# Kernel optimization log

Measured on AMD Instinct MI355X. Metric: run time of the kernel, lower is better.

## Reference

```python
import jax, jax.numpy as jnp
import numpy as np

SEQ_LEN = 8192
INPUT_SIZE = 1024
HIDDEN_SIZE = 2048


def setup_inputs() -> dict:
    key = jax.random.key(0)
    k_in, k_wz, k_wr, k_wh = jax.random.split(key, 4)
    concat = HIDDEN_SIZE + INPUT_SIZE
    return {
        "inputs": jax.random.normal(k_in, (SEQ_LEN, INPUT_SIZE), dtype=jnp.float32),
        "W_z": jax.random.normal(k_wz, (HIDDEN_SIZE, concat), dtype=jnp.float32) * 0.01,
        "b_z": jnp.zeros((HIDDEN_SIZE, 1), dtype=jnp.float32),
        "W_r": jax.random.normal(k_wr, (HIDDEN_SIZE, concat), dtype=jnp.float32) * 0.01,
        "b_r": jnp.zeros((HIDDEN_SIZE, 1), dtype=jnp.float32),
        "W_h": jax.random.normal(k_wh, (HIDDEN_SIZE, concat), dtype=jnp.float32) * 0.01,
        "b_h": jnp.zeros((HIDDEN_SIZE, 1), dtype=jnp.float32),
    }


def reference(inputs, W_z, b_z, W_r, b_r, W_h, b_h):
    # inputs: [T, I]; hidden state h: [H, 1] (batch size 1, column-vector form).
    H = W_z.shape[0]
    h0 = jnp.zeros((H, 1), dtype=inputs.dtype)

    def step(h_prev, x_t):
        x = x_t[:, None]  # [I, 1]
        concat = jnp.concatenate([h_prev, x], axis=0)  # [H+I, 1]
        z = jax.nn.sigmoid(W_z @ concat + b_z)
        r = jax.nn.sigmoid(W_r @ concat + b_r)
        concat_reset = jnp.concatenate([r * h_prev, x], axis=0)
        h_tilde = jnp.tanh(W_h @ concat_reset + b_h)
        h_t = (1.0 - z) * h_prev + z * h_tilde
        return h_t, h_t

    h_final, outputs = jax.lax.scan(step, h0, inputs)
    # outputs: [T, H, 1] (stack of the per-step hidden states the torch code collects in a list)
    return outputs, h_final
```

## Files before the change

kernel.cpp:

```cpp
#include <hip/hip_runtime.h>

#define SEQ  8192
#define HID  2048
#define INP  1024
#define CONC 3072
#define NBLK 256
#define RPB  8

typedef unsigned short u16;

__device__ __forceinline__ u16 f2bf(float f){
  unsigned u = __float_as_uint(f);
  u = (u + 0x7fffu + ((u >> 16) & 1u)) >> 16;
  return (u16)u;
}
__device__ __forceinline__ float bf2f(u16 s){ return __uint_as_float(((unsigned)s) << 16); }
__device__ __forceinline__ float bfl(unsigned p){ return __uint_as_float(p << 16); }
__device__ __forceinline__ float bfh(unsigned p){ return __uint_as_float(p & 0xffff0000u); }

__device__ __forceinline__ float cload(const float* p){
  return __hip_atomic_load(p, __ATOMIC_RELAXED, __HIP_MEMORY_SCOPE_AGENT);
}
__device__ __forceinline__ void cstore(float* p, float v){
  __hip_atomic_store(p, v, __ATOMIC_RELAXED, __HIP_MEMORY_SCOPE_AGENT);
}
__device__ __forceinline__ unsigned cloadu(const unsigned* p){
  return __hip_atomic_load(p, __ATOMIC_RELAXED, __HIP_MEMORY_SCOPE_AGENT);
}
__device__ __forceinline__ void cstoreu(unsigned* p, unsigned v){
  __hip_atomic_store(p, v, __ATOMIC_RELAXED, __HIP_MEMORY_SCOPE_AGENT);
}

__global__ __launch_bounds__(256) void gru_gemm(
    const float* __restrict__ X,
    const float* __restrict__ Wz, const float* __restrict__ Wr, const float* __restrict__ Wh,
    const float* __restrict__ bz, const float* __restrict__ br, const float* __restrict__ bh,
    u16* __restrict__ Uz, u16* __restrict__ Ur, u16* __restrict__ Uh)
{
  const int g = blockIdx.z;
  const float* W    = (g == 0) ? Wz : (g == 1) ? Wr : Wh;
  const float* bias = (g == 0) ? bz : (g == 1) ? br : bh;
  u16* U            = (g == 0) ? Uz : (g == 1) ? Ur : Uh;

  __shared__ __align__(16) float Xs[16][68];
  __shared__ __align__(16) float Ws[16][68];

  const int tid = threadIdx.x;
  const int tx = tid & 15, ty = tid >> 4;
  const int t0 = blockIdx.y * 64, i0 = blockIdx.x * 64;
  const int lrow = tid >> 2, lk = (tid & 3) * 4;

  const float* xsrc = X + (size_t)(t0 + lrow) * INP + lk;
  const float* wsrc = W + (size_t)(i0 + lrow) * CONC + HID + lk;

  float4 acc[4];
  acc[0] = acc[1] = acc[2] = acc[3] = make_float4(0.f, 0.f, 0.f, 0.f);

  for (int k0 = 0; k0 < INP; k0 += 16) {
    float4 xv = *(const float4*)(xsrc + k0);
    float4 wv = *(const float4*)(wsrc + k0);
    Xs[lk + 0][lrow] = xv.x; Xs[lk + 1][lrow] = xv.y;
    Xs[lk + 2][lrow] = xv.z; Xs[lk + 3][lrow] = xv.w;
    Ws[lk + 0][lrow] = wv.x; Ws[lk + 1][lrow] = wv.y;
    Ws[lk + 2][lrow] = wv.z; Ws[lk + 3][lrow] = wv.w;
    __syncthreads();
#pragma unroll
    for (int kk = 0; kk < 16; kk++) {
      float4 xa = *(const float4*)&Xs[kk][ty * 4];
      float4 wb = *(const float4*)&Ws[kk][tx * 4];
      acc[0].x = fmaf(xa.x, wb.x, acc[0].x); acc[0].y = fmaf(xa.x, wb.y, acc[0].y);
      acc[0].z = fmaf(xa.x, wb.z, acc[0].z); acc[0].w = fmaf(xa.x, wb.w, acc[0].w);
      acc[1].x = fmaf(xa.y, wb.x, acc[1].x); acc[1].y = fmaf(xa.y, wb.y, acc[1].y);
      acc[1].z = fmaf(xa.y, wb.z, acc[1].z); acc[1].w = fmaf(xa.y, wb.w, acc[1].w);
      acc[2].x = fmaf(xa.z, wb.x, acc[2].x); acc[2].y = fmaf(xa.z, wb.y, acc[2].y);
      acc[2].z = fmaf(xa.z, wb.z, acc[2].z); acc[2].w = fmaf(xa.z, wb.w, acc[2].w);
      acc[3].x = fmaf(xa.w, wb.x, acc[3].x); acc[3].y = fmaf(xa.w, wb.y, acc[3].y);
      acc[3].z = fmaf(xa.w, wb.z, acc[3].z); acc[3].w = fmaf(xa.w, wb.w, acc[3].w);
    }
    __syncthreads();
  }

  float4 bv = *(const float4*)(bias + i0 + tx * 4);
#pragma unroll
  for (int a = 0; a < 4; a++) {
    float4 v = acc[a];
    v.x += bv.x; v.y += bv.y; v.z += bv.z; v.w += bv.w;
    ushort4 o = make_ushort4(f2bf(v.x), f2bf(v.y), f2bf(v.z), f2bf(v.w));
    *(ushort4*)&U[(size_t)(t0 + ty * 4 + a) * HID + i0 + tx * 4] = o;
  }
}

__global__ __launch_bounds__(256, 1) void gru_rnn(
    const u16* __restrict__ U0, const u16* __restrict__ U1, const u16* __restrict__ U2,
    const float* __restrict__ Wz, const float* __restrict__ Wr, const float* __restrict__ Wh,
    float* __restrict__ h_g, float* __restrict__ rh_g,
    unsigned* __restrict__ hflag, unsigned* __restrict__ rhflag,
    float* __restrict__ out)
{
  __shared__ __align__(16) u16  w_s[3][RPB][HID];
  __shared__ __align__(16) float h_s[HID];
  __shared__ __align__(16) float rh_s[HID];
  __shared__ __align__(16) float hn_s[RPB];
  __shared__ u16  u_s[24];

  const int tid  = threadIdx.x;
  const int lane = tid & 63;
  const int wv   = tid >> 6;
  const int b    = blockIdx.x;
  const int i0   = b * RPB;

  {
    const float* Wm[3] = {Wz, Wr, Wh};
    const int c0 = tid * 8;
    for (int m = 0; m < 3; m++) {
      for (int r = 0; r < RPB; r++) {
        const float* src = Wm[m] + (size_t)(i0 + r) * CONC;
        u16* dst = &w_s[m][r][0];
        float4 v0 = *(const float4*)(src + c0);
        float4 v1 = *(const float4*)(src + c0 + 4);
        *(ushort4*)(dst + c0)     = make_ushort4(f2bf(v0.x), f2bf(v0.y), f2bf(v0.z), f2bf(v0.w));
        *(ushort4*)(dst + c0 + 4) = make_ushort4(f2bf(v1.x), f2bf(v1.y), f2bf(v1.z), f2bf(v1.w));
      }
    }
  }

  const u16* Ug[3] = {U0, U1, U2};
  const int pg = tid >> 3, pr = tid & 7;
  u16 u_next = 0;
  if (tid < 24) u_next = Ug[pg][(size_t)0 * HID + i0 + pr];

  float z_reg[2] = {0.f, 0.f};
  const int c0 = tid * 8;

  for (int t = 0; t < SEQ; ++t) {
    const float* hsrc = h_g + (size_t)(t & 1) * HID;
    float*       hdst = h_g + (size_t)((t + 1) & 1) * HID;
    float*       rhb  = rh_g + (size_t)(t & 1) * HID;

    while (cloadu(&hflag[tid]) < (unsigned)t) __builtin_amdgcn_s_sleep(1);
    asm volatile("" ::: "memory");
    {
      float hv8[8];
#pragma unroll
      for (int m = 0; m < 8; m++) hv8[m] = cload(&hsrc[c0 + m]);
#pragma unroll
      for (int m = 0; m < 8; m++) h_s[c0 + m] = hv8[m];
    }
    if (tid < 24) u_s[tid] = u_next;
    __syncthreads();
    if (tid < 24) {
      const int tn = (t + 1 < SEQ) ? (t + 1) : (SEQ - 1);
      u_next = Ug[pg][(size_t)tn * HID + i0 + pr];
    }

    float4 hv[8];
#pragma unroll
    for (int j = 0; j < 8; j++) hv[j] = ((const float4*)h_s)[j * 64 + lane];

#pragma unroll
    for (int q = 0; q < 2; q++) {
      const int r = wv * 2 + q;
      const u16* wrow = &w_s[1][r][0];
      float acc = 0.f;
#pragma unroll
      for (int j = 0; j < 8; j++) {
        uint2 p = ((const uint2*)wrow)[j * 64 + lane];
        float4 hh = hv[j];
        acc = fmaf(bfl(p.x), hh.x, acc);
        acc = fmaf(bfh(p.x), hh.y, acc);
        acc = fmaf(bfl(p.y), hh.z, acc);
        acc = fmaf(bfh(p.y), hh.w, acc);
      }
#pragma unroll
      for (int o = 32; o; o >>= 1) acc += __shfl_xor(acc, o);
      if (lane == 0) {
        const float a = acc + bf2f(u_s[8 + r]);
        const float s = 1.f / (1.f + __expf(-a));
        cstore(&rhb[i0 + r], s * h_s[i0 + r]);
      }
    }
    asm volatile("s_waitcnt vmcnt(0)" ::: "memory");
    __syncthreads();
    if (tid == 0) cstoreu(&rhflag[b], (unsigned)(t + 1));

#pragma unroll
    for (int q = 0; q < 2; q++) {
      const int r = wv * 2 + q;
      const u16* wrow = &w_s[0][r][0];
      float acc = 0.f;
#pragma unroll
      for (int j = 0; j < 8; j++) {
        uint2 p = ((const uint2*)wrow)[j * 64 + lane];
        float4 hh = hv[j];
        acc = fmaf(bfl(p.x), hh.x, acc);
        acc = fmaf(bfh(p.x), hh.y, acc);
        acc = fmaf(bfl(p.y), hh.z, acc);
        acc = fmaf(bfh(p.y), hh.w, acc);
      }
#pragma unroll
      for (int o = 32; o; o >>= 1) acc += __shfl_xor(acc, o);
      if (lane == 0) {
        const float a = acc + bf2f(u_s[0 + r]);
        z_reg[q] = 1.f / (1.f + __expf(-a));
      }
    }

    while (cloadu(&rhflag[tid]) < (unsigned)(t + 1)) __builtin_amdgcn_s_sleep(1);
    asm volatile("" ::: "memory");
    {
      float rv8[8];
#pragma unroll
      for (int m = 0; m < 8; m++) rv8[m] = cload(&rhb[c0 + m]);
#pragma unroll
      for (int m = 0; m < 8; m++) rh_s[c0 + m] = rv8[m];
    }
    __syncthreads();

    float4 rv[8];
#pragma unroll
    for (int j = 0; j < 8; j++) rv[j] = ((const float4*)rh_s)[j * 64 + lane];

#pragma unroll
    for (int q = 0; q < 2; q++) {
      const int r = wv * 2 + q;
      const u16* wrow = &w_s[2][r][0];
      float acc = 0.f;
#pragma unroll
      for (int j = 0; j < 8; j++) {
        uint2 p = ((const uint2*)wrow)[j * 64 + lane];
        float4 hh = rv[j];
        acc = fmaf(bfl(p.x), hh.x, acc);
        acc = fmaf(bfh(p.x), hh.y, acc);
        acc = fmaf(bfl(p.y), hh.z, acc);
        acc = fmaf(bfh(p.y), hh.w, acc);
      }
#pragma unroll
      for (int o = 32; o; o >>= 1) acc += __shfl_xor(acc, o);
      if (lane == 0) {
        const float a  = acc + bf2f(u_s[16 + r]);
        const float ht = tanhf(a);
        const float z  = z_reg[q];
        const int i = i0 + r;
        const float hn = (1.f - z) * h_s[i] + z * ht;
        hn_s[r] = hn;
        cstore(&hdst[i], hn);
      }
    }
    asm volatile("s_waitcnt vmcnt(0)" ::: "memory");
    __syncthreads();
    if (tid == 0) cstoreu(&hflag[b], (unsigned)(t + 1));
    if (tid < 2) {
      float4 v = ((const float4*)hn_s)[tid];
      *(float4*)&out[(size_t)t * HID + i0 + tid * 4] = v;
      if (t == SEQ - 1)
        *(float4*)&out[(size_t)SEQ * HID + i0 + tid * 4] = v;
    }
  }
}

extern "C" void kernel_launch(void* const* d_in, const int* in_sizes, int n_in,
                              void* d_out, int out_size, void* d_ws, size_t ws_size,
                              hipStream_t stream)
{
  const float* X  = (const float*)d_in[0];
  const float* Wz = (const float*)d_in[1];
  const float* bz = (const float*)d_in[2];
  const float* Wr = (const float*)d_in[3];
  const float* br = (const float*)d_in[4];
  const float* Wh = (const float*)d_in[5];
  const float* bh = (const float*)d_in[6];
  float* out = (float*)d_out;

  char* ws = (char*)d_ws;
  const size_t SZ_U = (size_t)SEQ * HID * sizeof(u16);
  u16* Uz = (u16*)(ws);
  u16* Ur = (u16*)(ws + SZ_U);
  u16* Uh = (u16*)(ws + 2 * SZ_U);
  float* h_g      = (float*)(ws + 3 * SZ_U);
  float* rh_g     = h_g + 2 * HID;
  unsigned* hflag  = (unsigned*)(rh_g + 2 * HID);
  unsigned* rhflag = hflag + NBLK;

  hipMemsetAsync(ws + 3 * SZ_U, 0, (size_t)4 * HID * 4 + 2 * NBLK * 4, stream);

  gru_gemm<<<dim3(HID / 64, SEQ / 64, 3), 256, 0, stream>>>(
      X, Wz, Wr, Wh, bz, br, bh, Uz, Ur, Uh);

  gru_rnn<<<dim3(NBLK), dim3(256), 0, stream>>>(
      Uz, Ur, Uh, Wz, Wr, Wh, h_g, rh_g, hflag, rhflag, out);
}
```

Before: 85.95 ms.

## Replace flat all-to-all flag polling with two-level hierarchical group barrier

```diff
diff --git a/kernel.cpp b/kernel.cpp
--- a/kernel.cpp
+++ b/kernel.cpp
@@ -6,6 +6,8 @@
 #define CONC 3072
 #define NBLK 256
 #define RPB  8
+#define GRP  32
+#define NG   8
 
 typedef unsigned short u16;
 
@@ -94,7 +96,8 @@
     const u16* __restrict__ U0, const u16* __restrict__ U1, const u16* __restrict__ U2,
     const float* __restrict__ Wz, const float* __restrict__ Wr, const float* __restrict__ Wh,
     float* __restrict__ h_g, float* __restrict__ rh_g,
-    unsigned* __restrict__ hflag, unsigned* __restrict__ rhflag,
+    unsigned* __restrict__ mfh, unsigned* __restrict__ mfr,
+    unsigned* __restrict__ gfh, unsigned* __restrict__ gfr,
     float* __restrict__ out)
 {
   __shared__ __align__(16) u16  w_s[3][RPB][HID];
@@ -108,6 +111,9 @@
   const int wv   = tid >> 6;
   const int b    = blockIdx.x;
   const int i0   = b * RPB;
+  const int grp  = b >> 5;
+  const int slot = b & 31;
+  const bool leader = (slot == 0);
 
   {
     const float* Wm[3] = {Wz, Wr, Wh};
@@ -130,21 +136,29 @@
   if (tid < 24) u_next = Ug[pg][(size_t)0 * HID + i0 + pr];
 
   float z_reg[2] = {0.f, 0.f};
-  const int c0 = tid * 8;
 
   for (int t = 0; t < SEQ; ++t) {
     const float* hsrc = h_g + (size_t)(t & 1) * HID;
     float*       hdst = h_g + (size_t)((t + 1) & 1) * HID;
     float*       rhb  = rh_g + (size_t)(t & 1) * HID;
 
-    while (cloadu(&hflag[tid]) < (unsigned)t) __builtin_amdgcn_s_sleep(1);
+    if (wv == 0) {
+      const unsigned tgt = (unsigned)t;
+      for (;;) {
+        unsigned v = cloadu(&gfh[lane & 7]);
+        if (__all((int)(v >= tgt))) break;
+        __builtin_amdgcn_s_sleep(1);
+      }
+    }
     asm volatile("" ::: "memory");
+    __syncthreads();
+
     {
       float hv8[8];
 #pragma unroll
-      for (int m = 0; m < 8; m++) hv8[m] = cload(&hsrc[c0 + m]);
-#pragma unroll
-      for (int m = 0; m < 8; m++) h_s[c0 + m] = hv8[m];
+      for (int m = 0; m < 8; m++) hv8[m] = cload(&hsrc[tid + m * 256]);
+#pragma unroll
+      for (int m = 0; m < 8; m++) h_s[tid + m * 256] = hv8[m];
     }
     if (tid < 24) u_s[tid] = u_next;
     __syncthreads();
@@ -181,7 +195,15 @@
     }
     asm volatile("s_waitcnt vmcnt(0)" ::: "memory");
     __syncthreads();
-    if (tid == 0) cstoreu(&rhflag[b], (unsigned)(t + 1));
+    if (tid == 0) cstoreu(&mfr[grp * 64 + slot], (unsigned)(t + 1));
+    if (leader && wv == 0) {
+      const unsigned tgt = (unsigned)(t + 1);
+      for (;;) {
+        unsigned v = cloadu(&mfr[grp * 64 + (lane & 31)]);
+        if (__all((int)(v >= tgt))) break;
+      }
+      if (lane == 0) cstoreu(&gfr[grp], tgt);
+    }
 
 #pragma unroll
     for (int q = 0; q < 2; q++) {
@@ -205,14 +227,23 @@
       }
     }
 
-    while (cloadu(&rhflag[tid]) < (unsigned)(t + 1)) __builtin_amdgcn_s_sleep(1);
+    if (wv == 0) {
+      const unsigned tgt = (unsigned)(t + 1);
+      for (;;) {
+        unsigned v = cloadu(&gfr[lane & 7]);
+        if (__all((int)(v >= tgt))) break;
+        __builtin_amdgcn_s_sleep(1);
+      }
+    }
     asm volatile("" ::: "memory");
+    __syncthreads();
+
     {
       float rv8[8];
 #pragma unroll
-      for (int m = 0; m < 8; m++) rv8[m] = cload(&rhb[c0 + m]);
-#pragma unroll
-      for (int m = 0; m < 8; m++) rh_s[c0 + m] = rv8[m];
+      for (int m = 0; m < 8; m++) rv8[m] = cload(&rhb[tid + m * 256]);
+#pragma unroll
+      for (int m = 0; m < 8; m++) rh_s[tid + m * 256] = rv8[m];
     }
     __syncthreads();
 
@@ -248,7 +279,15 @@
     }
     asm volatile("s_waitcnt vmcnt(0)" ::: "memory");
     __syncthreads();
-    if (tid == 0) cstoreu(&hflag[b], (unsigned)(t + 1));
+    if (tid == 0) cstoreu(&mfh[grp * 64 + slot], (unsigned)(t + 1));
+    if (leader && wv == 0) {
+      const unsigned tgt = (unsigned)(t + 1);
+      for (;;) {
+        unsigned v = cloadu(&mfh[grp * 64 + (lane & 31)]);
+        if (__all((int)(v >= tgt))) break;
+      }
+      if (lane == 0) cstoreu(&gfh[grp], tgt);
+    }
     if (tid < 2) {
       float4 v = ((const float4*)hn_s)[tid];
       *(float4*)&out[(size_t)t * HID + i0 + tid * 4] = v;
@@ -276,16 +315,19 @@
   u16* Uz = (u16*)(ws);
   u16* Ur = (u16*)(ws + SZ_U);
   u16* Uh = (u16*)(ws + 2 * SZ_U);
-  float* h_g      = (float*)(ws + 3 * SZ_U);
-  float* rh_g     = h_g + 2 * HID;
-  unsigned* hflag  = (unsigned*)(rh_g + 2 * HID);
-  unsigned* rhflag = hflag + NBLK;
-
-  hipMemsetAsync(ws + 3 * SZ_U, 0, (size_t)4 * HID * 4 + 2 * NBLK * 4, stream);
+  float* h_g   = (float*)(ws + 3 * SZ_U);
+  float* rh_g  = h_g + 2 * HID;
+  unsigned* mfh = (unsigned*)(rh_g + 2 * HID);
+  unsigned* mfr = mfh + NG * 64;
+  unsigned* gfh = mfr + NG * 64;
+  unsigned* gfr = gfh + 16;
+
+  const size_t ctrl_bytes = (size_t)4 * HID * 4 + (2 * NG * 64 + 32) * 4;
+  hipMemsetAsync(ws + 3 * SZ_U, 0, ctrl_bytes, stream);
 
   gru_gemm<<<dim3(HID / 64, SEQ / 64, 3), 256, 0, stream>>>(
       X, Wz, Wr, Wh, bz, br, bh, Uz, Ur, Uh);
 
   gru_rnn<<<dim3(NBLK), dim3(256), 0, stream>>>(
-      Uz, Ur, Uh, Wz, Wr, Wh, h_g, rh_g, hflag, rhflag, out);
-}
+      Uz, Ur, Uh, Wz, Wr, Wh, h_g, rh_g, mfh, mfr, gfh, gfr, out);
+}
```

Result: faster. 78.64 ms (-8.5%).
